# Kernel optimization log

Measured on AMD Instinct MI355X. Metric: run time of the kernel, lower is better.

Reference implementation:

```python
import jax, jax.numpy as jnp
import numpy as np

D_IN = 1024
D_OUT = 1024
N_HEADS = 16
HEAD_DIM = D_OUT // N_HEADS


def setup_inputs() -> dict:
    key = jax.random.key(0)
    ks = jax.random.split(key, 6)
    s = 0.02
    x = jax.random.normal(ks[0], (4, 2048, D_IN), dtype=jnp.float32)
    Wq = jax.random.normal(ks[1], (D_IN, D_OUT), dtype=jnp.float32) * s
    Wk = jax.random.normal(ks[2], (D_IN, D_OUT), dtype=jnp.float32) * s
    Wv = jax.random.normal(ks[3], (D_IN, D_OUT), dtype=jnp.float32) * s
    Wo = jax.random.normal(ks[4], (D_OUT, D_OUT), dtype=jnp.float32) * s
    bo = jax.random.normal(ks[5], (D_OUT,), dtype=jnp.float32) * s
    return {"x": x, "Wq": Wq, "Wk": Wk, "Wv": Wv, "Wo": Wo, "bo": bo}


def reference(x, Wq, Wk, Wv, Wo, bo):
    B, S, _ = x.shape
    # projections -> [B, H, S, Dh]
    def split_heads(t):
        return t.reshape(B, S, N_HEADS, HEAD_DIM).transpose(0, 2, 1, 3)
    q = split_heads(x @ Wq)
    k = split_heads(x @ Wk)
    v = split_heads(x @ Wv)
    scores = jnp.einsum('bhqd,bhkd->bhqk', q, k)  # [B,H,S,S]
    causal = jnp.triu(jnp.ones((S, S), dtype=bool), k=1)
    scores = jnp.where(causal, -jnp.inf, scores)
    attn = jax.nn.softmax(scores / np.sqrt(HEAD_DIM).astype(np.float32), axis=-1)
    ctx = jnp.einsum('bhqk,bhkd->bhqd', attn, v)  # [B,H,S,Dh]
    ctx = ctx.transpose(0, 2, 1, 3).reshape(B, S, D_OUT)
    return ctx @ Wo + bo
```

## Files before the change

kernel.cpp:

```cpp
#include <hip/hip_runtime.h>
#include <hip/hip_bf16.h>
#include <math.h>

typedef __attribute__((ext_vector_type(8))) short bf16x8;
typedef __attribute__((ext_vector_type(4))) float f32x4;
typedef __attribute__((ext_vector_type(16))) float f32x16;
typedef __attribute__((ext_vector_type(4))) unsigned int u32x4;

static constexpr int Mtot = 8192;
static constexpr int Dmod = 1024;
static constexpr int SEQ  = 2048;
static constexpr int NH   = 16;
static constexpr int DH   = 64;

static constexpr float QSCALE = 0.18033688011112042f;

__device__ __forceinline__ unsigned short f2bf(float x) {
    unsigned int u = __float_as_uint(x);
    u += 0x7fff + ((u >> 16) & 1);
    return (unsigned short)(u >> 16);
}

__device__ __forceinline__ void gload_lds16(const void* g, void* l) {
    __builtin_amdgcn_global_load_lds(
        (const __attribute__((address_space(1))) unsigned int*)g,
        (__attribute__((address_space(3))) unsigned int*)l, 16, 0, 0);
}

__global__ __launch_bounds__(256)
void cvt_bf16(const float* __restrict__ in, unsigned short* __restrict__ out, int n4) {
    int i = blockIdx.x * blockDim.x + threadIdx.x;
    const int stride = gridDim.x * blockDim.x;
    for (; i < n4; i += stride) {
        float4 v = ((const float4*)in)[i];
        ushort4 o;
        o.x = f2bf(v.x); o.y = f2bf(v.y); o.z = f2bf(v.z); o.w = f2bf(v.w);
        ((ushort4*)out)[i] = o;
    }
}

__global__ __launch_bounds__(256)
void transpose_cvt4(const float* __restrict__ W0, const float* __restrict__ W1,
                    const float* __restrict__ W2, const float* __restrict__ W3,
                    unsigned short* __restrict__ T0, unsigned short* __restrict__ T1,
                    unsigned short* __restrict__ T2, unsigned short* __restrict__ T3) {
    __shared__ float tile[64][68];
    const int z = blockIdx.z;
    const float* W = z == 0 ? W0 : z == 1 ? W1 : z == 2 ? W2 : W3;
    unsigned short* Wt = z == 0 ? T0 : z == 1 ? T1 : z == 2 ? T2 : T3;

    const int n0 = blockIdx.x * 64, k0 = blockIdx.y * 64;
    const int t = threadIdx.x;
    const int r = t >> 4, c4 = (t & 15) * 4;
#pragma unroll
    for (int i = 0; i < 4; ++i) {
        float4 v = *(const float4*)&W[(size_t)(k0 + r + i * 16) * Dmod + n0 + c4];
        tile[c4 + 0][r + i * 16] = v.x;
        tile[c4 + 1][r + i * 16] = v.y;
        tile[c4 + 2][r + i * 16] = v.z;
        tile[c4 + 3][r + i * 16] = v.w;
    }
    __syncthreads();
#pragma unroll
    for (int i = 0; i < 4; ++i) {
        ushort4 o;
        o.x = f2bf(tile[r + i * 16][c4 + 0]);
        o.y = f2bf(tile[r + i * 16][c4 + 1]);
        o.z = f2bf(tile[r + i * 16][c4 + 2]);
        o.w = f2bf(tile[r + i * 16][c4 + 3]);
        *(ushort4*)&Wt[(size_t)(n0 + r + i * 16) * Dmod + k0 + c4] = o;
    }
}

template<int MODE>
__global__ __launch_bounds__(512)
void gemm256(const unsigned short* __restrict__ A,
             const unsigned short* __restrict__ Bw,
             const float* __restrict__ bias,
             unsigned short* __restrict__ Qb,
             unsigned short* __restrict__ Kb,
             unsigned short* __restrict__ Vtb,
             float* __restrict__ Fout) {
    __shared__ __align__(16) char lds[131072];

    const int id  = blockIdx.x;
    const int xcd = id & 7, idx = id >> 3;
    constexpr int NTN = MODE == 0 ? 12 : 4;
    const int mt = xcd * 4 + idx / NTN;
    const int nt = idx % NTN;
    const int m0 = mt * 256, n0 = nt * 256;

    const int t = threadIdx.x;
    const int wid = t >> 6, l = t & 63;
    const int wm = wid >> 2, wn = wid & 3;
    const int r16 = l & 15, g = l >> 4;

    auto stage = [&](const unsigned short* src, int row0, int kt, int kh, int regionOff) {
        char* dst = lds + regionOff + wid * 1024;
#pragma unroll
        for (int r = 0; r < 2; ++r) {
            const int o  = r * 8192 + t * 16;
            const int lg = o ^ (((o >> 7) & 3) << 4);
            gload_lds16((const char*)src + (size_t)(row0 + (lg >> 6)) * 2048
                            + kt * 128 + kh * 64 + (lg & 63),
                        dst + r * 8192);
        }
    };

    f32x4 acc[8][4];
    const f32x4 z = {0.f, 0.f, 0.f, 0.f};
#pragma unroll
    for (int i = 0; i < 8; ++i)
#pragma unroll
        for (int j = 0; j < 4; ++j) acc[i][j] = z;

    stage(A,  m0, 0, 0, 0);
    stage(Bw, n0, 0, 0, 16384);
    stage(A,  m0, 0, 1, 32768);
    stage(Bw, n0, 0, 1, 49152);

    const int arow0 = wm * 128 + r16;
    const int brow0 = wn * 64 + r16;
    const int gb = g * 16;

    for (int kt = 0; kt < 16; ++kt) {
        const int buf  = (kt & 1) << 16;
        const int nbuf = buf ^ 65536;
        const int ktn  = kt < 15 ? kt + 1 : 15;
        bf16x8 af[8], bv[2];

        stage(A, m0, ktn, 0, nbuf);
        asm volatile("s_waitcnt vmcnt(6)" ::: "memory");
        __builtin_amdgcn_s_barrier();
#pragma unroll
        for (int mi = 0; mi < 8; ++mi) {
            const int row = arow0 + mi * 16;
            af[mi] = *(const bf16x8*)(lds + buf
                      + ((row * 64 + gb) ^ (((row >> 1) & 3) << 4)));
        }
#pragma unroll
        for (int ni = 0; ni < 2; ++ni) {
            const int row = brow0 + ni * 16;
            bv[ni] = *(const bf16x8*)(lds + buf + 16384
                      + ((row * 64 + gb) ^ (((row >> 1) & 3) << 4)));
        }
        asm volatile("s_waitcnt lgkmcnt(0)" ::: "memory");
        __builtin_amdgcn_sched_barrier(0);
        __builtin_amdgcn_s_setprio(1);
#pragma unroll
        for (int mi = 0; mi < 8; ++mi)
#pragma unroll
            for (int ni = 0; ni < 2; ++ni)
                acc[mi][ni] = __builtin_amdgcn_mfma_f32_16x16x32_bf16(
                    af[mi], bv[ni], acc[mi][ni], 0, 0, 0);
        __builtin_amdgcn_s_setprio(0);

        stage(Bw, n0, ktn, 0, nbuf + 16384);
#pragma unroll
        for (int ni = 0; ni < 2; ++ni) {
            const int row = brow0 + (2 + ni) * 16;
            bv[ni] = *(const bf16x8*)(lds + buf + 16384
                      + ((row * 64 + gb) ^ (((row >> 1) & 3) << 4)));
        }
        asm volatile("s_waitcnt lgkmcnt(0)" ::: "memory");
        __builtin_amdgcn_sched_barrier(0);
        __builtin_amdgcn_s_setprio(1);
#pragma unroll
        for (int mi = 0; mi < 8; ++mi)
#pragma unroll
            for (int ni = 0; ni < 2; ++ni)
                acc[mi][2 + ni] = __builtin_amdgcn_mfma_f32_16x16x32_bf16(
                    af[mi], bv[ni], acc[mi][2 + ni], 0, 0, 0);
        __builtin_amdgcn_s_setprio(0);

        stage(A, m0, ktn, 1, nbuf + 32768);
        asm volatile("s_waitcnt vmcnt(6)" ::: "memory");
        __builtin_amdgcn_s_barrier();
#pragma unroll
        for (int mi = 0; mi < 8; ++mi) {
            const int row = arow0 + mi * 16;
            af[mi] = *(const bf16x8*)(lds + buf + 32768
                      + ((row * 64 + gb) ^ (((row >> 1) & 3) << 4)));
        }
#pragma unroll
        for (int ni = 0; ni < 2; ++ni) {
            const int row = brow0 + ni * 16;
            bv[ni] = *(const bf16x8*)(lds + buf + 49152
                      + ((row * 64 + gb) ^ (((row >> 1) & 3) << 4)));
        }
        asm volatile("s_waitcnt lgkmcnt(0)" ::: "memory");
        __builtin_amdgcn_sched_barrier(0);
        __builtin_amdgcn_s_setprio(1);
#pragma unroll
        for (int mi = 0; mi < 8; ++mi)
#pragma unroll
            for (int ni = 0; ni < 2; ++ni)
                acc[mi][ni] = __builtin_amdgcn_mfma_f32_16x16x32_bf16(
                    af[mi], bv[ni], acc[mi][ni], 0, 0, 0);
        __builtin_amdgcn_s_setprio(0);

        stage(Bw, n0, ktn, 1, nbuf + 49152);
#pragma unroll
        for (int ni = 0; ni < 2; ++ni) {
            const int row = brow0 + (2 + ni) * 16;
            bv[ni] = *(const bf16x8*)(lds + buf + 49152
                      + ((row * 64 + gb) ^ (((row >> 1) & 3) << 4)));
        }
        asm volatile("s_waitcnt lgkmcnt(0)" ::: "memory");
        __builtin_amdgcn_sched_barrier(0);
        __builtin_amdgcn_s_setprio(1);
#pragma unroll
        for (int mi = 0; mi < 8; ++mi)
#pragma unroll
            for (int ni = 0; ni < 2; ++ni)
                acc[mi][2 + ni] = __builtin_amdgcn_mfma_f32_16x16x32_bf16(
                    af[mi], bv[ni], acc[mi][2 + ni], 0, 0, 0);
        __builtin_amdgcn_s_setprio(0);
    }

    if constexpr (MODE == 0) {
        const int region = n0 >> 10;
        if (region <= 1) {
            unsigned short* outp = region ? Kb : Qb;
            const float qs = region == 0 ? QSCALE : 1.0f;
#pragma unroll
            for (int mi = 0; mi < 8; ++mi) {
                const int mrow = m0 + wm * 128 + mi * 16 + g * 4;
#pragma unroll
                for (int ni = 0; ni < 4; ++ni) {
                    const int ncol = (n0 & 1023) + wn * 64 + ni * 16 + r16;
#pragma unroll
                    for (int reg = 0; reg < 4; ++reg)
                        outp[(size_t)(mrow + reg) * Dmod + ncol] = f2bf(acc[mi][ni][reg] * qs);
                }
            }
        } else {
#pragma unroll
            for (int mi = 0; mi < 8; ++mi) {
                const int mrow = m0 + wm * 128 + mi * 16 + g * 4;
                const int bidx = mrow >> 11, s = mrow & 2047;
#pragma unroll
                for (int ni = 0; ni < 4; ++ni) {
                    const int n = (n0 & 1023) + wn * 64 + ni * 16 + r16;
                    const int bh = bidx * NH + (n >> 6), d = n & 63;
                    ushort4 o;
                    o.x = f2bf(acc[mi][ni][0]); o.y = f2bf(acc[mi][ni][1]);
                    o.z = f2bf(acc[mi][ni][2]); o.w = f2bf(acc[mi][ni][3]);
                    *(ushort4*)&Vtb[((size_t)bh * DH + d) * SEQ + s] = o;
                }
            }
        }
    } else {
        float bb[4];
#pragma unroll
        for (int ni = 0; ni < 4; ++ni)
            bb[ni] = bias[n0 + wn * 64 + ni * 16 + r16];
#pragma unroll
        for (int mi = 0; mi < 8; ++mi) {
            const int mrow = m0 + wm * 128 + mi * 16 + g * 4;
#pragma unroll
            for (int ni = 0; ni < 4; ++ni) {
                const int ncol = n0 + wn * 64 + ni * 16 + r16;
#pragma unroll
                for (int reg = 0; reg < 4; ++reg)
                    Fout[(size_t)(mrow + reg) * Dmod + ncol] = acc[mi][ni][reg] + bb[ni];
            }
        }
    }
}

__global__ __launch_bounds__(256, 2)
void attn_mfma(const unsigned short* __restrict__ Qg,
               const unsigned short* __restrict__ Kg,
               const unsigned short* __restrict__ Vtg,
               unsigned short* __restrict__ Ctx) {
    __shared__ __align__(16) short Ks[2][64 * 64];
    __shared__ __align__(16) short Vs[2][64 * 64];
    __shared__ float sm[4][32];

    const int id   = blockIdx.x;
    const int bh   = ((id >> 6) << 3) | (id & 7);
    const int pidx = (id >> 3) & 7;
    const int b = bh >> 4, h = bh & 15;
    const int t = threadIdx.x, wid = t >> 6, l = t & 63;
    const int lo = l & 31, hi = l >> 5;
    const int srow8 = t >> 3, scolb = (t & 7) * 16;

    auto stageKV = [&](int jt, int buf) {
        const int k0s = jt * 64;
#pragma unroll
        for (int c = 0; c < 2; ++c) {
            const int row = c * 32 + srow8;
            const int swz = scolb ^ ((row & 7) << 4);
            gload_lds16((const char*)Kg + ((size_t)(b * SEQ + k0s + row) * Dmod + h * DH) * 2 + swz,
                        (char*)&Ks[buf][0] + c * 4096 + wid * 1024);
            gload_lds16((const char*)Vtg + ((size_t)(bh * DH + row) * SEQ + k0s) * 2 + swz,
                        (char*)&Vs[buf][0] + c * 4096 + wid * 1024);
        }
    };

    int cur = 0;
    for (int pass = 0; pass < 2; ++pass) {
        const int qt = pass ? pidx : 15 - pidx;
        const int q0 = qt * 128;
        const int qw0 = q0 + wid * 32;
        const int qg = qw0 + lo;

        bf16x8 bq[4];
#pragma unroll
        for (int dc = 0; dc < 4; ++dc)
            bq[dc] = *(const bf16x8*)&Qg[(size_t)(b * SEQ + qg) * Dmod + h * DH + dc * 16 + 8 * hi];

        stageKV(0, cur);

        float m_run = -1e30f, l_run = 0.f;
        f32x16 oacc[2];
#pragma unroll
        for (int nb = 0; nb < 2; ++nb)
#pragma unroll
            for (int r = 0; r < 16; ++r) oacc[nb][r] = 0.f;

        __syncthreads();

        const int jmax = 2 * qt + 1;
        for (int jt = 0; jt <= jmax; ++jt) {
            if (jt < jmax) stageKV(jt + 1, cur ^ 1);
            const char* Kc = (const char*)&Ks[cur][0];
            const char* Vc = (const char*)&Vs[cur][0];
            const bool diag = (jt >= 2 * qt);

#pragma unroll
            for (int c32 = 0; c32 < 2; ++c32) {
                const int krow = c32 * 32 + lo;
                const int kswz = (krow & 7) << 4;
                bf16x8 ak[4];
#pragma unroll
                for (int dc = 0; dc < 4; ++dc)
                    ak[dc] = *(const bf16x8*)(Kc + krow * 128 + ((dc * 32 + 16 * hi) ^ kswz));
                f32x16 st;
#pragma unroll
                for (int r = 0; r < 16; ++r) st[r] = 0.f;
                __builtin_amdgcn_s_setprio(1);
#pragma unroll
                for (int dc = 0; dc < 4; ++dc)
                    st = __builtin_amdgcn_mfma_f32_32x32x16_bf16(ak[dc], bq[dc], st, 0, 0, 0);
                __builtin_amdgcn_s_setprio(0);

                if (diag) {
                    const int kvb = jt * 64 + c32 * 32 + 4 * hi;
#pragma unroll
                    for (int r = 0; r < 16; ++r) {
                        const int kvg = kvb + (r & 3) + 8 * (r >> 2);
                        if (kvg > qg) st[r] = -1e30f;
                    }
                }

                float pmax = st[0];
#pragma unroll
                for (int r = 1; r < 16; ++r) pmax = fmaxf(pmax, st[r]);
                pmax = fmaxf(pmax, __shfl_xor(pmax, 32));

                if (!__all(pmax <= m_run + 8.f)) {
                    const float mnew = fmaxf(m_run, pmax);
                    const float sc = exp2f(m_run - mnew);
                    l_run *= sc;
                    m_run = mnew;
                    if (l < 32) sm[wid][lo] = sc;
                    asm volatile("s_waitcnt lgkmcnt(0)" ::: "memory");
#pragma unroll
                    for (int rq = 0; rq < 4; ++rq) {
                        const f32x4 s4 = *(const f32x4*)&sm[wid][8 * rq + 4 * hi];
#pragma unroll
                        for (int e = 0; e < 4; ++e) {
                            oacc[0][rq * 4 + e] *= s4[e];
                            oacc[1][rq * 4 + e] *= s4[e];
                        }
                    }
                }

                float p[16];
                float rsum = 0.f;
#pragma unroll
                for (int r = 0; r < 16; ++r) { p[r] = exp2f(st[r] - m_run); rsum += p[r]; }
                rsum += __shfl_xor(rsum, 32);
                l_run += rsum;

#pragma unroll
                for (int kb = 0; kb < 2; ++kb) {
                    unsigned int x, zz, y, w;
                    asm("v_cvt_pk_bf16_f32 %0, %1, %2" : "=v"(x)  : "v"(p[kb*8+0]), "v"(p[kb*8+1]));
                    asm("v_cvt_pk_bf16_f32 %0, %1, %2" : "=v"(zz) : "v"(p[kb*8+2]), "v"(p[kb*8+3]));
                    asm("v_cvt_pk_bf16_f32 %0, %1, %2" : "=v"(y)  : "v"(p[kb*8+4]), "v"(p[kb*8+5]));
                    asm("v_cvt_pk_bf16_f32 %0, %1, %2" : "=v"(w)  : "v"(p[kb*8+6]), "v"(p[kb*8+7]));
                    asm volatile("v_permlane32_swap_b32 %0, %1" : "+v"(x),  "+v"(y));
                    asm volatile("v_permlane32_swap_b32 %0, %1" : "+v"(zz), "+v"(w));
                    u32x4 aw; aw[0] = x; aw[1] = zz; aw[2] = y; aw[3] = w;
                    const bf16x8 paf = __builtin_bit_cast(bf16x8, aw);

                    const int vbyte = c32 * 64 + kb * 32 + 16 * hi;
                    const int row0 = lo, row1 = 32 + lo;
                    const bf16x8 vb0 = *(const bf16x8*)(Vc + row0 * 128 + (vbyte ^ ((row0 & 7) << 4)));
                    const bf16x8 vb1 = *(const bf16x8*)(Vc + row1 * 128 + (vbyte ^ ((row1 & 7) << 4)));

                    __builtin_amdgcn_s_setprio(1);
                    oacc[0] = __builtin_amdgcn_mfma_f32_32x32x16_bf16(paf, vb0, oacc[0], 0, 0, 0);
                    oacc[1] = __builtin_amdgcn_mfma_f32_32x32x16_bf16(paf, vb1, oacc[1], 0, 0, 0);
                    __builtin_amdgcn_s_setprio(0);
                }
            }
            __syncthreads();
            cur ^= 1;
        }

        if (l < 32) sm[wid][lo] = l_run;
        asm volatile("s_waitcnt lgkmcnt(0)" ::: "memory");
#pragma unroll
        for (int rq = 0; rq < 4; ++rq) {
            const f32x4 lv = *(const f32x4*)&sm[wid][8 * rq + 4 * hi];
#pragma unroll
            for (int e = 0; e < 4; ++e) {
                const float inv = 1.0f / lv[e];
                const int qrow = qw0 + 8 * rq + 4 * hi + e;
                const size_t rb = (size_t)(b * SEQ + qrow) * Dmod + h * DH + lo;
                Ctx[rb]      = f2bf(oacc[0][rq * 4 + e] * inv);
                Ctx[rb + 32] = f2bf(oacc[1][rq * 4 + e] * inv);
            }
        }
    }
}

extern "C" void kernel_launch(void* const* d_in, const int* in_sizes, int n_in,
                              void* d_out, int out_size, void* d_ws, size_t ws_size,
                              hipStream_t stream) {
    const float* x  = (const float*)d_in[0];
    const float* Wq = (const float*)d_in[1];
    const float* Wk = (const float*)d_in[2];
    const float* Wv = (const float*)d_in[3];
    const float* Wo = (const float*)d_in[4];
    const float* bo = (const float*)d_in[5];
    float* out = (float*)d_out;

    const size_t MD = (size_t)Mtot * Dmod;
    const size_t DD = (size_t)Dmod * Dmod;
    unsigned short* xb  = (unsigned short*)d_ws;
    unsigned short* wtq = xb  + MD;
    unsigned short* wtk = wtq + DD;
    unsigned short* wtv = wtk + DD;
    unsigned short* wto = wtv + DD;
    unsigned short* Qb  = wto + DD;
    unsigned short* Kb  = Qb  + MD;
    unsigned short* Vtb = Kb  + MD;
    unsigned short* Cx  = Vtb + MD;

    cvt_bf16<<<2048, 256, 0, stream>>>(x, xb, (int)(MD / 4));
    transpose_cvt4<<<dim3(16, 16, 4), 256, 0, stream>>>(Wq, Wk, Wv, Wo,
                                                        wtq, wtk, wtv, wto);

    gemm256<0><<<384, 512, 0, stream>>>(xb, wtq, nullptr, Qb, Kb, Vtb, nullptr);

    attn_mfma<<<512, 256, 0, stream>>>(Qb, Kb, Vtb, Cx);

    gemm256<1><<<128, 512, 0, stream>>>(Cx, wto, bo, nullptr, nullptr, nullptr, out);
}
```

Before: 190.6 us.

## Split attention KV loop across two blocks and merge partials

Each (batch, head, q-tile pair) is now handled by two blocks that take alternating KV tiles (even/odd), doubling the grid from 512 to 1024 blocks. Each block writes unnormalized bf16 partial outputs plus its running max and sum, and a new merge kernel combines the two partials with log-sum-exp weights into the context tensor. The goal is more parallelism and occupancy across CUs. The cost is an extra kernel launch, extra global traffic for the partials, and bf16 rounding of the unnormalized partial outputs.

```diff
diff --git a/kernel.cpp b/kernel.cpp
--- a/kernel.cpp
+++ b/kernel.cpp
@@ -19,6 +19,10 @@
     unsigned int u = __float_as_uint(x);
     u += 0x7fff + ((u >> 16) & 1);
     return (unsigned short)(u >> 16);
+}
+
+__device__ __forceinline__ float bf2f(short s) {
+    return __uint_as_float(((unsigned int)(unsigned short)s) << 16);
 }
 
 __device__ __forceinline__ void gload_lds16(const void* g, void* l) {
@@ -273,14 +277,18 @@
 void attn_mfma(const unsigned short* __restrict__ Qg,
                const unsigned short* __restrict__ Kg,
                const unsigned short* __restrict__ Vtg,
-               unsigned short* __restrict__ Ctx) {
+               unsigned short* __restrict__ pO,
+               float* __restrict__ pML) {
     __shared__ __align__(16) short Ks[2][64 * 64];
     __shared__ __align__(16) short Vs[2][64 * 64];
     __shared__ float sm[4][32];
 
     const int id   = blockIdx.x;
-    const int bh   = ((id >> 6) << 3) | (id & 7);
-    const int pidx = (id >> 3) & 7;
+    const int xcd  = id & 7;
+    const int bh   = ((id >> 7) << 3) | xcd;
+    const int mid  = (id >> 3) & 15;
+    const int pidx = mid >> 1;
+    const int par  = mid & 1;
     const int b = bh >> 4, h = bh & 15;
     const int t = threadIdx.x, wid = t >> 6, l = t & 63;
     const int lo = l & 31, hi = l >> 5;
@@ -311,7 +319,7 @@
         for (int dc = 0; dc < 4; ++dc)
             bq[dc] = *(const bf16x8*)&Qg[(size_t)(b * SEQ + qg) * Dmod + h * DH + dc * 16 + 8 * hi];
 
-        stageKV(0, cur);
+        stageKV(par, cur);
 
         float m_run = -1e30f, l_run = 0.f;
         f32x16 oacc[2];
@@ -323,8 +331,8 @@
         __syncthreads();
 
         const int jmax = 2 * qt + 1;
-        for (int jt = 0; jt <= jmax; ++jt) {
-            if (jt < jmax) stageKV(jt + 1, cur ^ 1);
+        for (int jt = par; jt <= jmax; jt += 2) {
+            if (jt + 2 <= jmax) stageKV(jt + 2, cur ^ 1);
             const char* Kc = (const char*)&Ks[cur][0];
             const char* Vc = (const char*)&Vs[cur][0];
             const bool diag = (jt >= 2 * qt);
@@ -351,7 +359,7 @@
 #pragma unroll
                     for (int r = 0; r < 16; ++r) {
                         const int kvg = kvb + (r & 3) + 8 * (r >> 2);
-                        if (kvg > qg) st[r] = -1e30f;
+                        if (kvg > qg) st[r] = -INFINITY;
                     }
                 }
 
@@ -412,21 +420,45 @@
             cur ^= 1;
         }
 
-        if (l < 32) sm[wid][lo] = l_run;
-        asm volatile("s_waitcnt lgkmcnt(0)" ::: "memory");
+        if (hi == 0)
+            ((float2*)pML)[(size_t)(par * 64 + bh) * SEQ + qg] = make_float2(m_run, l_run);
+        const size_t pbase = (size_t)(par * 64 + bh) * SEQ;
 #pragma unroll
         for (int rq = 0; rq < 4; ++rq) {
-            const f32x4 lv = *(const f32x4*)&sm[wid][8 * rq + 4 * hi];
 #pragma unroll
             for (int e = 0; e < 4; ++e) {
-                const float inv = 1.0f / lv[e];
                 const int qrow = qw0 + 8 * rq + 4 * hi + e;
-                const size_t rb = (size_t)(b * SEQ + qrow) * Dmod + h * DH + lo;
-                Ctx[rb]      = f2bf(oacc[0][rq * 4 + e] * inv);
-                Ctx[rb + 32] = f2bf(oacc[1][rq * 4 + e] * inv);
+                unsigned short* pr = &pO[(pbase + qrow) * 64];
+                pr[lo]      = f2bf(oacc[0][rq * 4 + e]);
+                pr[lo + 32] = f2bf(oacc[1][rq * 4 + e]);
             }
         }
     }
+}
+
+__global__ __launch_bounds__(256)
+void attn_merge(const unsigned short* __restrict__ pO,
+                const float* __restrict__ pML,
+                unsigned short* __restrict__ Ctx) {
+    const int gid = blockIdx.x * 256 + threadIdx.x;
+    const int row = gid >> 3;
+    const int d8  = (gid & 7) * 8;
+    const float2 ml0 = ((const float2*)pML)[row];
+    const float2 ml1 = ((const float2*)pML)[131072 + row];
+    const float m  = fmaxf(ml0.x, ml1.x);
+    float w0 = exp2f(ml0.x - m), w1 = exp2f(ml1.x - m);
+    const float inv = 1.0f / fmaxf(ml0.y * w0 + ml1.y * w1, 1e-30f);
+    w0 *= inv; w1 *= inv;
+    const bf16x8 o0 = *(const bf16x8*)&pO[(size_t)row * 64 + d8];
+    const bf16x8 o1 = *(const bf16x8*)&pO[((size_t)131072 + row) * 64 + d8];
+    const int bh = row >> 11, q = row & 2047;
+    unsigned short* dst = &Ctx[((size_t)((bh >> 4) * SEQ + q)) * Dmod + (bh & 15) * DH + d8];
+    unsigned short r8[8];
+#pragma unroll
+    for (int j = 0; j < 8; ++j)
+        r8[j] = f2bf(bf2f(o0[j]) * w0 + bf2f(o1[j]) * w1);
+    *(ushort4*)dst       = make_ushort4(r8[0], r8[1], r8[2], r8[3]);
+    *(ushort4*)(dst + 4) = make_ushort4(r8[4], r8[5], r8[6], r8[7]);
 }
 
 extern "C" void kernel_launch(void* const* d_in, const int* in_sizes, int n_in,
@@ -452,13 +484,17 @@
     unsigned short* Vtb = Kb  + MD;
     unsigned short* Cx  = Vtb + MD;
 
+    unsigned short* pO  = Cx + MD;
+    float*          pML = (float*)(pO + (size_t)2 * 64 * SEQ * 64);
+
     cvt_bf16<<<2048, 256, 0, stream>>>(x, xb, (int)(MD / 4));
     transpose_cvt4<<<dim3(16, 16, 4), 256, 0, stream>>>(Wq, Wk, Wv, Wo,
                                                         wtq, wtk, wtv, wto);
 
     gemm256<0><<<384, 512, 0, stream>>>(xb, wtq, nullptr, Qb, Kb, Vtb, nullptr);
 
-    attn_mfma<<<512, 256, 0, stream>>>(Qb, Kb, Vtb, Cx);
+    attn_mfma<<<1024, 256, 0, stream>>>(Qb, Kb, Vtb, pO, pML);
+    attn_merge<<<4096, 256, 0, stream>>>(pO, pML, Cx);
 
     gemm256<1><<<128, 512, 0, stream>>>(Cx, wto, bo, nullptr, nullptr, nullptr, out);
 }
```

Result: no change. 193.4 us (+1.5%).
